# Kernel optimization log

Measured on AMD Instinct MI355X. Metric: run time of the kernel, lower is better.

The kernel has to match this reference:

```python
import jax, jax.numpy as jnp
import numpy as np
from jax import lax

EPS = 2.220446049250313e-16  # np.finfo(np.float64).eps
HALF_LOG_2PI = 0.9189385332046727


def setup_inputs() -> dict:
    N, M, K = 262144, 32, 16
    key = jax.random.key(0)
    kx, kmu, ksig = jax.random.split(key, 3)
    X = jax.random.normal(kx, (N, M), dtype=jnp.float32)
    wk0_logits = jnp.ones((1, K), dtype=jnp.float32)
    W_logits = jnp.ones((M, K, K), dtype=jnp.float32)
    mu = jax.random.uniform(kmu, (M, K, K), dtype=jnp.float32, minval=-4.0, maxval=4.0)
    pre_sigma = jax.random.uniform(ksig, (M, K, K), dtype=jnp.float32, minval=0.0, maxval=5.0)
    return {"X": X, "wk0_logits": wk0_logits, "W_logits": W_logits, "mu": mu, "pre_sigma": pre_sigma}


def reference(X, wk0_logits, W_logits, mu, pre_sigma):
    N, M = X.shape
    K = wk0_logits.shape[1]
    wk0 = jax.nn.softmax(wk0_logits, axis=1)            # (1, K)
    # tf.nn.softmax(W_logits[i], axis=0) over all i == softmax over axis=1 of (M,K,K)
    logW = jax.nn.log_softmax(W_logits, axis=1)          # (M, K, K)
    sigma = jax.nn.softplus(pre_sigma)                   # (M, K, K)
    log_sigma = jnp.log(sigma)

    def step(prod, inputs):
        logW_i, mu_i, sigma_i, log_sigma_i, x_i = inputs  # (K,K)x4, (N,)
        z = (x_i[:, None, None] - mu_i) / sigma_i          # (N, K, K)
        log_prob = -0.5 * z * z - log_sigma_i - HALF_LOG_2PI
        result = jnp.exp(logW_i + log_prob)                # (N, K, K)
        # prod @ result^T per sample
        prod = jnp.einsum('nij,nkj->nik', prod, result)
        return prod, None

    prod0 = jnp.broadcast_to(jnp.eye(K, dtype=X.dtype), (N, K, K))
    prod, _ = lax.scan(step, prod0, (logW, mu, sigma, log_sigma, X.T))
    # squeeze(wk0 @ prod, axis=1) -> (N, K); sum over K -> (N,)
    likelihoods = jnp.sum(jnp.einsum('k,nkj->nj', wk0[0], prod), axis=1)
    return jnp.log(likelihoods + EPS)
```

## Files before the change

kernel.cpp:

```cpp
#include <hip/hip_runtime.h>
#include <math.h>

typedef __attribute__((ext_vector_type(4))) float f32x4;
typedef __attribute__((ext_vector_type(4))) short s16x4;

#define LOG2E   1.4426950408889634f
#define EPSV    2.220446049250313e-16f
#define HLOG2PI 0.9189385332046727f

#define MAGICC  12599160.0f

static __device__ __forceinline__ float fexp2(float x) {
  return __builtin_amdgcn_exp2f(x);
}

static __device__ __forceinline__ unsigned pk_bf16t(float f0, float f1) {
  return __builtin_amdgcn_perm(__builtin_bit_cast(unsigned, f1),
                               __builtin_bit_cast(unsigned, f0), 0x07060302u);
}
static __device__ __forceinline__ unsigned pk_lo16_2(float u0, float u1) {
  return __builtin_amdgcn_perm(__builtin_bit_cast(unsigned, u1),
                               __builtin_bit_cast(unsigned, u0), 0x05040100u);
}

static __device__ __forceinline__ float rdlane(float v, int lane) {
  return __builtin_bit_cast(float,
      __builtin_amdgcn_readlane(__builtin_bit_cast(int, v), lane));
}

__global__ void tt_prep(const float* __restrict__ Wl,
                        const float* __restrict__ mu,
                        const float* __restrict__ ps,
                        float* __restrict__ abc, int M) {
  int g = blockIdx.x * blockDim.x + threadIdx.x;
  if (g >= M * 64) return;
  int m = g >> 6;
  int k = (g >> 2) & 15;
  int q = g & 3;
  const float SC = 128.0f * LOG2E;
  float av[4], bv[4], cv[4];
#pragma unroll
  for (int i = 0; i < 4; ++i) {
    int j = q * 4 + i;
    int base = m * 256 + j;
    float mx = -INFINITY;
    for (int kk = 0; kk < 16; ++kk) mx = fmaxf(mx, Wl[base + kk * 16]);
    float s = 0.f;
    for (int kk = 0; kk < 16; ++kk) s += expf(Wl[base + kk * 16] - mx);
    float lse = mx + logf(s);
    int idx = m * 256 + k * 16 + j;
    float logw = Wl[idx] - lse;
    float p  = ps[idx];
    float sg = (p > 20.f) ? p : log1pf(expf(p));
    float inv  = 1.0f / sg;
    float inv2 = inv * inv;
    float muv  = mu[idx];
    av[i] = SC * (logw - logf(sg) - HLOG2PI - 0.5f * muv * muv * inv2) + MAGICC;
    bv[i] = SC * (muv * inv2);
    cv[i] = SC * (-0.5f * inv2);
  }
  f32x4* o = (f32x4*)abc + (long)g * 3;
  o[0] = (f32x4){av[0], av[1], av[2], av[3]};
  o[1] = (f32x4){bv[0], bv[1], bv[2], bv[3]};
  o[2] = (f32x4){cv[0], cv[1], cv[2], cv[3]};
}

__global__ __launch_bounds__(256, 3)
void tt_main32(const float* __restrict__ X,
               const float* __restrict__ wk0_logits,
               const float* __restrict__ abc,
               float* __restrict__ out, int N) {
  const int l = (int)(threadIdx.x & 63u);
  const int wave = __builtin_amdgcn_readfirstlane((int)(threadIdx.x >> 6));
  const int c = l & 15;
  const int q = l >> 4;

  long nb = ((long)blockIdx.x * 4 + wave) * 8;
  if (nb > (long)N - 8) nb = (long)N - 8;

  float wl = wk0_logits[c];
  float mx = wl;
#pragma unroll
  for (int d = 1; d < 16; d <<= 1) mx = fmaxf(mx, __shfl_xor(mx, d, 64));
  float ew = fexp2((wl - mx) * LOG2E);
  float sw = ew;
#pragma unroll
  for (int d = 1; d < 16; d <<= 1) sw += __shfl_xor(sw, d, 64);
  float w0 = ew / sw;

  f32x4 q0;
#pragma unroll
  for (int i = 0; i < 4; ++i) q0[i] = __shfl(w0, 4 * q + i, 64);

  unsigned Qx[8], Qy[8];
#pragma unroll
  for (int s = 0; s < 8; ++s) {
    Qx[s] = pk_bf16t(q0[0], q0[1]);
    Qy[s] = pk_bf16t(q0[2], q0[3]);
  }

  const float* Xn = X + nb * 32;
  float4 xq = *(const float4*)(Xn + l * 4);

  const int lofs = (c * 4 + q) * 12;
  f32x4 pa = *(const f32x4*)(abc + lofs);
  f32x4 pb = *(const f32x4*)(abc + lofs + 4);
  f32x4 pc = *(const f32x4*)(abc + lofs + 8);
  const f32x4 zero = (f32x4){0.f, 0.f, 0.f, 0.f};
  const s16x4 clmp = (s16x4){0x0080, 0x0080, 0x0080, 0x0080};

  for (int m4 = 0; m4 < 32; m4 += 4) {
    const int sb = m4 >> 2;
#pragma unroll
    for (int t = 0; t < 4; ++t) {
      const int step = m4 + t;
      const int ns = (step < 31) ? step + 1 : 31;
      const float* Pn = abc + (long)ns * 768 + lofs;
      f32x4 na = *(const f32x4*)(Pn);
      f32x4 nb4 = *(const f32x4*)(Pn + 4);
      f32x4 nc = *(const f32x4*)(Pn + 8);

#pragma unroll
      for (int s = 0; s < 8; ++s) {
        float xs = rdlane(((const float*)&xq)[t], sb + s * 8);
        float u0 = fmaf(fmaf(pc[0], xs, pb[0]), xs, pa[0]);
        float u1 = fmaf(fmaf(pc[1], xs, pb[1]), xs, pa[1]);
        float u2 = fmaf(fmaf(pc[2], xs, pb[2]), xs, pa[2]);
        float u3 = fmaf(fmaf(pc[3], xs, pb[3]), xs, pa[3]);
        uint2 at;
        at.x = pk_lo16_2(u0, u1);
        at.y = pk_lo16_2(u2, u3);
        s16x4 af = __builtin_elementwise_max(__builtin_bit_cast(s16x4, at), clmp);
        s16x4 bf = __builtin_bit_cast(s16x4, (uint2){Qx[s], Qy[s]});
        f32x4 D = __builtin_amdgcn_mfma_f32_16x16x16bf16_1k(af, bf, zero,
                                                            0, 0, 0);
        Qx[s] = pk_bf16t(D[0], D[1]);
        Qy[s] = pk_bf16t(D[2], D[3]);
      }
      pa = na; pb = nb4; pc = nc;
    }
  }

  float res = 0.0f;
#pragma unroll
  for (int s = 0; s < 8; ++s) {
    float v0 = __builtin_bit_cast(float, Qx[s] << 16);
    float v1 = __builtin_bit_cast(float, Qx[s] & 0xFFFF0000u);
    float v2 = __builtin_bit_cast(float, Qy[s] << 16);
    float v3 = __builtin_bit_cast(float, Qy[s] & 0xFFFF0000u);
    float t = (v0 + v1) + (v2 + v3);
    t += __shfl_xor(t, 16, 64);
    t += __shfl_xor(t, 32, 64);
    if (l == s) res = t;
  }
  if (l < 8) {
    long n0 = nb + l;
    if (n0 < (long)N) out[n0] = logf(res + EPSV);
  }
}

__global__ __launch_bounds__(256, 3)
void tt_main_gen(const float* __restrict__ X,
                 const float* __restrict__ wk0_logits,
                 const float* __restrict__ abc,
                 float* __restrict__ out, int N, int M) {
  const int l = (int)(threadIdx.x & 63u);
  const int wave = __builtin_amdgcn_readfirstlane((int)(threadIdx.x >> 6));
  const int c = l & 15;
  const int q = l >> 4;

  long nb = ((long)blockIdx.x * 4 + wave) * 8;
  if (nb > (long)N - 8) nb = (long)N - 8;

  float wl = wk0_logits[c];
  float mx = wl;
#pragma unroll
  for (int d = 1; d < 16; d <<= 1) mx = fmaxf(mx, __shfl_xor(mx, d, 64));
  float ew = fexp2((wl - mx) * LOG2E);
  float sw = ew;
#pragma unroll
  for (int d = 1; d < 16; d <<= 1) sw += __shfl_xor(sw, d, 64);
  float w0 = ew / sw;

  f32x4 q0;
#pragma unroll
  for (int i = 0; i < 4; ++i) q0[i] = __shfl(w0, 4 * q + i, 64);
  unsigned Qx[8], Qy[8];
#pragma unroll
  for (int s = 0; s < 8; ++s) {
    Qx[s] = pk_bf16t(q0[0], q0[1]);
    Qy[s] = pk_bf16t(q0[2], q0[3]);
  }

  const float* Xn = X + nb * (long)M;
  const f32x4* Pm = (const f32x4*)abc + (c * 4 + q) * 3;
  f32x4 pa = Pm[0], pb = Pm[1], pc = Pm[2];
  const f32x4 zero = (f32x4){0.f, 0.f, 0.f, 0.f};
  const s16x4 clmp = (s16x4){0x0080, 0x0080, 0x0080, 0x0080};

  for (int m = 0; m < M; ++m) {
    f32x4 qa, qb4, qc;
    const f32x4* Pn = Pm + 192;
    bool more = (m + 1 < M);
    if (more) { qa = Pn[0]; qb4 = Pn[1]; qc = Pn[2]; }
#pragma unroll
    for (int s = 0; s < 8; ++s) {
      float xs = Xn[(long)s * M + m];
      float u0 = fmaf(fmaf(pc[0], xs, pb[0]), xs, pa[0]);
      float u1 = fmaf(fmaf(pc[1], xs, pb[1]), xs, pa[1]);
      float u2 = fmaf(fmaf(pc[2], xs, pb[2]), xs, pa[2]);
      float u3 = fmaf(fmaf(pc[3], xs, pb[3]), xs, pa[3]);
      uint2 at;
      at.x = pk_lo16_2(u0, u1);
      at.y = pk_lo16_2(u2, u3);
      s16x4 af = __builtin_elementwise_max(__builtin_bit_cast(s16x4, at), clmp);
      s16x4 bf = __builtin_bit_cast(s16x4, (uint2){Qx[s], Qy[s]});
      f32x4 D = __builtin_amdgcn_mfma_f32_16x16x16bf16_1k(af, bf, zero,
                                                          0, 0, 0);
      Qx[s] = pk_bf16t(D[0], D[1]);
      Qy[s] = pk_bf16t(D[2], D[3]);
    }
    if (more) { pa = qa; pb = qb4; pc = qc; Pm = Pn; }
  }

  float res = 0.0f;
#pragma unroll
  for (int s = 0; s < 8; ++s) {
    float v0 = __builtin_bit_cast(float, Qx[s] << 16);
    float v1 = __builtin_bit_cast(float, Qx[s] & 0xFFFF0000u);
    float v2 = __builtin_bit_cast(float, Qy[s] << 16);
    float v3 = __builtin_bit_cast(float, Qy[s] & 0xFFFF0000u);
    float t = (v0 + v1) + (v2 + v3);
    t += __shfl_xor(t, 16, 64);
    t += __shfl_xor(t, 32, 64);
    if (l == s) res = t;
  }
  if (l < 8) {
    long n0 = nb + l;
    if (n0 < (long)N) out[n0] = logf(res + EPSV);
  }
}

extern "C" void kernel_launch(void* const* d_in, const int* in_sizes, int n_in,
                              void* d_out, int out_size, void* d_ws, size_t ws_size,
                              hipStream_t stream) {
  const float* X   = (const float*)d_in[0];
  const float* wk0 = (const float*)d_in[1];
  const float* Wl  = (const float*)d_in[2];
  const float* mu  = (const float*)d_in[3];
  const float* ps  = (const float*)d_in[4];
  int K = in_sizes[1];
  int M = in_sizes[2] / (K * K);
  int N = in_sizes[0] / M;
  float* abc = (float*)d_ws;

  tt_prep<<<(M * 64 + 255) / 256, 256, 0, stream>>>(Wl, mu, ps, abc, M);
  int blocks = (int)((N + 31) / 32);
  if (M == 32) {
    tt_main32<<<blocks, 256, 0, stream>>>(X, wk0, abc, (float*)d_out, N);
  } else {
    tt_main_gen<<<blocks, 256, 0, stream>>>(X, wk0, abc, (float*)d_out, N, M);
  }
}
```

Before: 334.0 us.

## Process 16 samples per wave and use packed FP32 FMAs

Each wave in the M=32 kernel now carries 16 independent sample chains instead of 8, loading two X tiles and halving the block count. The quadratic-exponent evaluation is written with 2-wide float vectors so the compiler can emit packed FMA instructions, and the launch-bounds occupancy hints are raised. The intent is more independent MFMA chains per wave to hide the MFMA dependency latency and fewer VALU ops per step. The cost is higher register pressure from the 16 accumulators under a tighter occupancy target, which could cause spills.

After: 316.9 us. -5.1%, faster.

```diff
diff --git a/kernel.cpp b/kernel.cpp
--- a/kernel.cpp
+++ b/kernel.cpp
@@ -2,6 +2,7 @@
 #include <math.h>
 
 typedef __attribute__((ext_vector_type(4))) float f32x4;
+typedef __attribute__((ext_vector_type(2))) float f32x2;
 typedef __attribute__((ext_vector_type(4))) short s16x4;
 
 #define LOG2E   1.4426950408889634f
@@ -18,9 +19,9 @@
   return __builtin_amdgcn_perm(__builtin_bit_cast(unsigned, f1),
                                __builtin_bit_cast(unsigned, f0), 0x07060302u);
 }
-static __device__ __forceinline__ unsigned pk_lo16_2(float u0, float u1) {
-  return __builtin_amdgcn_perm(__builtin_bit_cast(unsigned, u1),
-                               __builtin_bit_cast(unsigned, u0), 0x05040100u);
+static __device__ __forceinline__ unsigned pk_lo16(f32x2 u) {
+  return __builtin_amdgcn_perm(__builtin_bit_cast(uint2, u).y,
+                               __builtin_bit_cast(uint2, u).x, 0x05040100u);
 }
 
 static __device__ __forceinline__ float rdlane(float v, int lane) {
@@ -65,7 +66,7 @@
   o[2] = (f32x4){cv[0], cv[1], cv[2], cv[3]};
 }
 
-__global__ __launch_bounds__(256, 3)
+__global__ __launch_bounds__(256, 6)
 void tt_main32(const float* __restrict__ X,
                const float* __restrict__ wk0_logits,
                const float* __restrict__ abc,
@@ -75,8 +76,8 @@
   const int c = l & 15;
   const int q = l >> 4;
 
-  long nb = ((long)blockIdx.x * 4 + wave) * 8;
-  if (nb > (long)N - 8) nb = (long)N - 8;
+  long nb = ((long)blockIdx.x * 4 + wave) * 16;
+  if (nb > (long)N - 16) nb = (long)N - 16;
 
   float wl = wk0_logits[c];
   float mx = wl;
@@ -92,15 +93,15 @@
 #pragma unroll
   for (int i = 0; i < 4; ++i) q0[i] = __shfl(w0, 4 * q + i, 64);
 
-  unsigned Qx[8], Qy[8];
-#pragma unroll
-  for (int s = 0; s < 8; ++s) {
-    Qx[s] = pk_bf16t(q0[0], q0[1]);
-    Qy[s] = pk_bf16t(q0[2], q0[3]);
-  }
+  unsigned sx = pk_bf16t(q0[0], q0[1]);
+  unsigned sy = pk_bf16t(q0[2], q0[3]);
+  unsigned Qx[16], Qy[16];
+#pragma unroll
+  for (int s = 0; s < 16; ++s) { Qx[s] = sx; Qy[s] = sy; }
 
   const float* Xn = X + nb * 32;
-  float4 xq = *(const float4*)(Xn + l * 4);
+  float4 xq0 = *(const float4*)(Xn + l * 4);
+  float4 xq1 = *(const float4*)(Xn + 256 + l * 4);
 
   const int lofs = (c * 4 + q) * 12;
   f32x4 pa = *(const f32x4*)(abc + lofs);
@@ -120,16 +121,22 @@
       f32x4 nb4 = *(const f32x4*)(Pn + 4);
       f32x4 nc = *(const f32x4*)(Pn + 8);
 
-#pragma unroll
-      for (int s = 0; s < 8; ++s) {
-        float xs = rdlane(((const float*)&xq)[t], sb + s * 8);
-        float u0 = fmaf(fmaf(pc[0], xs, pb[0]), xs, pa[0]);
-        float u1 = fmaf(fmaf(pc[1], xs, pb[1]), xs, pa[1]);
-        float u2 = fmaf(fmaf(pc[2], xs, pb[2]), xs, pa[2]);
-        float u3 = fmaf(fmaf(pc[3], xs, pb[3]), xs, pa[3]);
+      f32x2 c01 = {pc[0], pc[1]}, c23 = {pc[2], pc[3]};
+      f32x2 b01 = {pb[0], pb[1]}, b23 = {pb[2], pb[3]};
+      f32x2 a01 = {pa[0], pa[1]}, a23 = {pa[2], pa[3]};
+
+#pragma unroll
+      for (int s = 0; s < 16; ++s) {
+        float xsrc = (s < 8) ? ((const float*)&xq0)[t] : ((const float*)&xq1)[t];
+        float xs = rdlane(xsrc, sb + (s & 7) * 8);
+        f32x2 xx = {xs, xs};
+        f32x2 u01 = __builtin_elementwise_fma(
+                        __builtin_elementwise_fma(c01, xx, b01), xx, a01);
+        f32x2 u23 = __builtin_elementwise_fma(
+                        __builtin_elementwise_fma(c23, xx, b23), xx, a23);
         uint2 at;
-        at.x = pk_lo16_2(u0, u1);
-        at.y = pk_lo16_2(u2, u3);
+        at.x = pk_lo16(u01);
+        at.y = pk_lo16(u23);
         s16x4 af = __builtin_elementwise_max(__builtin_bit_cast(s16x4, at), clmp);
         s16x4 bf = __builtin_bit_cast(s16x4, (uint2){Qx[s], Qy[s]});
         f32x4 D = __builtin_amdgcn_mfma_f32_16x16x16bf16_1k(af, bf, zero,
@@ -143,7 +150,7 @@
 
   float res = 0.0f;
 #pragma unroll
-  for (int s = 0; s < 8; ++s) {
+  for (int s = 0; s < 16; ++s) {
     float v0 = __builtin_bit_cast(float, Qx[s] << 16);
     float v1 = __builtin_bit_cast(float, Qx[s] & 0xFFFF0000u);
     float v2 = __builtin_bit_cast(float, Qy[s] << 16);
@@ -153,13 +160,13 @@
     t += __shfl_xor(t, 32, 64);
     if (l == s) res = t;
   }
-  if (l < 8) {
+  if (l < 16) {
     long n0 = nb + l;
     if (n0 < (long)N) out[n0] = logf(res + EPSV);
   }
 }
 
-__global__ __launch_bounds__(256, 3)
+__global__ __launch_bounds__(256, 4)
 void tt_main_gen(const float* __restrict__ X,
                  const float* __restrict__ wk0_logits,
                  const float* __restrict__ abc,
@@ -206,13 +213,17 @@
 #pragma unroll
     for (int s = 0; s < 8; ++s) {
       float xs = Xn[(long)s * M + m];
-      float u0 = fmaf(fmaf(pc[0], xs, pb[0]), xs, pa[0]);
-      float u1 = fmaf(fmaf(pc[1], xs, pb[1]), xs, pa[1]);
-      float u2 = fmaf(fmaf(pc[2], xs, pb[2]), xs, pa[2]);
-      float u3 = fmaf(fmaf(pc[3], xs, pb[3]), xs, pa[3]);
+      f32x2 xx = {xs, xs};
+      f32x2 c01 = {pc[0], pc[1]}, c23 = {pc[2], pc[3]};
+      f32x2 b01 = {pb[0], pb[1]}, b23 = {pb[2], pb[3]};
+      f32x2 a01 = {pa[0], pa[1]}, a23 = {pa[2], pa[3]};
+      f32x2 u01 = __builtin_elementwise_fma(
+                      __builtin_elementwise_fma(c01, xx, b01), xx, a01);
+      f32x2 u23 = __builtin_elementwise_fma(
+                      __builtin_elementwise_fma(c23, xx, b23), xx, a23);
       uint2 at;
-      at.x = pk_lo16_2(u0, u1);
-      at.y = pk_lo16_2(u2, u3);
+      at.x = pk_lo16(u01);
+      at.y = pk_lo16(u23);
       s16x4 af = __builtin_elementwise_max(__builtin_bit_cast(s16x4, at), clmp);
       s16x4 bf = __builtin_bit_cast(s16x4, (uint2){Qx[s], Qy[s]});
       f32x4 D = __builtin_amdgcn_mfma_f32_16x16x16bf16_1k(af, bf, zero,
@@ -255,10 +266,11 @@
   float* abc = (float*)d_ws;
 
   tt_prep<<<(M * 64 + 255) / 256, 256, 0, stream>>>(Wl, mu, ps, abc, M);
-  int blocks = (int)((N + 31) / 32);
   if (M == 32) {
+    int blocks = (int)((N + 63) / 64);
     tt_main32<<<blocks, 256, 0, stream>>>(X, wk0, abc, (float*)d_out, N);
   } else {
+    int blocks = (int)((N + 31) / 32);
     tt_main_gen<<<blocks, 256, 0, stream>>>(X, wk0, abc, (float*)d_out, N, M);
   }
 }
```
